# Kernel tuning notes

Hardware: AMD Instinct MI355X
Metric: run time of the kernel (lower is better)

The kernel has to match this reference:

```python
import jax, jax.numpy as jnp
import numpy as np

B, L, D_ENC = 32, 512, 512
STEPS = 32
E_DIM = 128      # embedding_dim
A_DIM = 256      # attention_dim
H = 512          # hidden_size
VOCAB = 32000


def _linear(x, W, b):
    return x @ W.T + b


def setup_inputs() -> dict:
    key = jax.random.key(0)
    ks = jax.random.split(key, 12)
    s = lambda fan_in: 1.0 / np.sqrt(fan_in)
    return {
        "encoder_outputs": jax.random.normal(ks[0], (B, L, D_ENC), dtype=jnp.float32),
        "target_seq": jax.random.randint(ks[1], (B, STEPS), 0, VOCAB, dtype=jnp.int64),
        "pos_embedding": jax.random.normal(ks[2], (STEPS, E_DIM), dtype=jnp.float32),
        "dec_proj_W": jax.random.uniform(ks[3], (A_DIM, E_DIM), minval=-s(E_DIM), maxval=s(E_DIM)),
        "dec_proj_b": jnp.zeros((A_DIM,), jnp.float32),
        "enc_proj_W": jax.random.uniform(ks[4], (A_DIM, D_ENC), minval=-s(D_ENC), maxval=s(D_ENC)),
        "enc_proj_b": jnp.zeros((A_DIM,), jnp.float32),
        "attn_score_W": jax.random.uniform(ks[5], (1, A_DIM), minval=-s(A_DIM), maxval=s(A_DIM)),
        "attn_score_b": jnp.zeros((1,), jnp.float32),
        "hidden_proj_W": jax.random.uniform(ks[6], (H, E_DIM), minval=-s(E_DIM), maxval=s(E_DIM)),
        "hidden_proj_b": jnp.zeros((H,), jnp.float32),
        "fc_out_W": jax.random.uniform(ks[7], (VOCAB, H + D_ENC), minval=-s(H + D_ENC), maxval=s(H + D_ENC)),
        "fc_out_b": jnp.zeros((VOCAB,), jnp.float32),
    }


def reference(encoder_outputs, target_seq, pos_embedding,
              dec_proj_W, dec_proj_b, enc_proj_W, enc_proj_b,
              attn_score_W, attn_score_b, hidden_proj_W, hidden_proj_b,
              fc_out_W, fc_out_b):
    batch = encoder_outputs.shape[0]
    steps = target_seq.shape[1]
    # [B, L, A]
    enc_proj = _linear(encoder_outputs, enc_proj_W, enc_proj_b)
    # [B, S, E]  (dropout=0 in eval)
    pos_emb = jnp.broadcast_to(pos_embedding[:steps][None], (batch, steps, pos_embedding.shape[1]))
    # [B, S, A]
    dec_query = _linear(pos_emb, dec_proj_W, dec_proj_b)
    # additive attention: [B, S, L, A]
    combined = jnp.tanh(enc_proj[:, None, :, :] + dec_query[:, :, None, :])
    # score reduction to scalar: [B, S, L]
    attn_scores = jnp.einsum('bsla,a->bsl', combined, attn_score_W[0]) + attn_score_b[0]
    attn_weights = jax.nn.softmax(attn_scores, axis=2)
    # context: [B, S, D_enc]
    context = jnp.einsum('bsl,bld->bsd', attn_weights, encoder_outputs)
    hidden = _linear(pos_emb, hidden_proj_W, hidden_proj_b)  # [B, S, H]
    logits = _linear(jnp.concatenate([hidden, context], axis=-1), fc_out_W, fc_out_b)
    return logits
```

## Files before the change

### kernel.cpp

```cpp
#include <hip/hip_runtime.h>
#include <hip/hip_bf16.h>
#include <stdint.h>

typedef __attribute__((ext_vector_type(4))) float f32x4;
typedef __attribute__((ext_vector_type(8))) short short8;

#define B_   32
#define L_   512
#define DE_  512
#define S_   32
#define ED_  128
#define AD_  256
#define HD_  512
#define VOC_ 32000
#define M_   1024

__device__ __forceinline__ unsigned short f2bf(float f){
  union { float f; unsigned int u; } v; v.f = f;
  unsigned int u = v.u;
  unsigned int r = (u + 0x7FFFu + ((u >> 16) & 1u)) >> 16;
  return (unsigned short)r;
}

__device__ __forceinline__ float bf2f(unsigned short u){
  union { unsigned int u; float f; } v; v.u = ((unsigned int)u) << 16;
  return v.f;
}

__device__ __forceinline__ float tanh_fast(float x){
  float t = __expf(2.0f * x);
  return (t - 1.0f) * __builtin_amdgcn_rcpf(t + 1.0f);
}

__device__ __forceinline__ void gl_lds16(const void* g, void* l){
  __builtin_amdgcn_global_load_lds(
      (const __attribute__((address_space(1))) unsigned int*)g,
      (__attribute__((address_space(3))) unsigned int*)l, 16, 0, 0);
}

extern "C" __global__ void __launch_bounds__(256)
k_cvt(const float* __restrict__ src, unsigned short* __restrict__ dst, int n4){
  int stride = gridDim.x * 256;
  for (int i = blockIdx.x * 256 + threadIdx.x; i < n4; i += stride){
    f32x4 v = ((const f32x4*)src)[i];
    ushort4 o;
    o.x = f2bf(v[0]); o.y = f2bf(v[1]); o.z = f2bf(v[2]); o.w = f2bf(v[3]);
    ((ushort4*)dst)[i] = o;
  }
}

extern "C" __global__ void __launch_bounds__(256)
k_small(const float* __restrict__ pos, const float* __restrict__ dW, const float* __restrict__ db,
        const float* __restrict__ hW, const float* __restrict__ hb,
        float* __restrict__ dq, unsigned short* __restrict__ hbf){
  int t = blockIdx.x * 256 + threadIdx.x;
  if (t < S_ * AD_){
    int s = t >> 8, a = t & 255;
    const float* p = pos + s * ED_;
    const float* wrow = dW + a * ED_;
    float acc = db[a];
    #pragma unroll 4
    for (int e = 0; e < ED_; ++e) acc += p[e] * wrow[e];
    dq[t] = acc;
  } else if (t < S_ * AD_ + S_ * HD_){
    int u = t - S_ * AD_;
    int s = u >> 9, h = u & 511;
    const float* p = pos + s * ED_;
    const float* wrow = hW + h * ED_;
    float acc = hb[h];
    #pragma unroll 4
    for (int e = 0; e < ED_; ++e) acc += p[e] * wrow[e];
    hbf[u] = f2bf(acc);
  }
}

extern "C" __global__ void __launch_bounds__(256)
k_gemm_encp(const unsigned short* __restrict__ A, const unsigned short* __restrict__ Bt,
            const float* __restrict__ bias, unsigned short* __restrict__ C){
  __shared__ unsigned short As[128 * 32];
  __shared__ unsigned short Bs[128 * 32];
  int bm = blockIdx.x >> 1, bn = blockIdx.x & 1;
  int tid = threadIdx.x, wid = tid >> 6, lane = tid & 63;
  int fr = lane & 15, fq = lane >> 4;
  int wm = wid >> 1, wn = wid & 1;
  f32x4 acc[4][4];
  #pragma unroll
  for (int i = 0; i < 4; ++i)
    #pragma unroll
    for (int j = 0; j < 4; ++j) acc[i][j] = (f32x4)0.0f;

  for (int k0 = 0; k0 < 512; k0 += 32){
    __syncthreads();
    #pragma unroll
    for (int i = 0; i < 2; ++i){
      int seg = wid * 2 + i;
      int row = seg * 16 + (lane >> 2);
      int col = (lane & 3) * 8;
      gl_lds16(A  + (size_t)(bm * 128 + row) * 512 + k0 + col, &As[seg * 512]);
      gl_lds16(Bt + (size_t)(bn * 128 + row) * 512 + k0 + col, &Bs[seg * 512]);
    }
    __syncthreads();
    short8 a[4], b[4];
    #pragma unroll
    for (int mf = 0; mf < 4; ++mf) a[mf] = *(const short8*)&As[(wm * 64 + mf * 16 + fr) * 32 + fq * 8];
    #pragma unroll
    for (int nf = 0; nf < 4; ++nf) b[nf] = *(const short8*)&Bs[(wn * 64 + nf * 16 + fr) * 32 + fq * 8];
    #pragma unroll
    for (int mf = 0; mf < 4; ++mf)
      #pragma unroll
      for (int nf = 0; nf < 4; ++nf)
        acc[mf][nf] = __builtin_amdgcn_mfma_f32_16x16x32_bf16(a[mf], b[nf], acc[mf][nf], 0, 0, 0);
  }
  #pragma unroll
  for (int mf = 0; mf < 4; ++mf){
    int row = bm * 128 + wm * 64 + mf * 16 + fq * 4;
    #pragma unroll
    for (int nf = 0; nf < 4; ++nf){
      int col = bn * 128 + wn * 64 + nf * 16 + fr;
      float bv = bias[col];
      #pragma unroll
      for (int j = 0; j < 4; ++j)
        C[(size_t)(row + j) * 256 + col] = f2bf(acc[mf][nf][j] + bv);
    }
  }
}

extern "C" __global__ void __launch_bounds__(256)
k_attn(const unsigned short* __restrict__ encp, const float* __restrict__ dq,
       const float* __restrict__ vW, float* __restrict__ wgt){
  int idx = blockIdx.x;
  int wg = (idx & 7) * 128 + (idx >> 3);
  int b = wg >> 5, s = wg & 31;
  int tid = threadIdx.x, wid = tid >> 6, lane = tid & 63;
  int half = lane >> 5, a0 = (lane & 31) * 8;
  __shared__ float sc[512];
  __shared__ float redm[4], reds[4];
  f32x4 dqa = *(const f32x4*)&dq[s * AD_ + a0];
  f32x4 dqb = *(const f32x4*)&dq[s * AD_ + a0 + 4];
  f32x4 va  = *(const f32x4*)&vW[a0];
  f32x4 vb  = *(const f32x4*)&vW[a0 + 4];
  for (int it = 0; it < 64; ++it){
    int l = wid * 128 + it * 2 + half;
    short8 e8 = *(const short8*)&encp[((size_t)(b * 512 + l)) * 256 + a0];
    float p = 0.0f;
    #pragma unroll
    for (int j = 0; j < 4; ++j) p += tanh_fast(bf2f((unsigned short)e8[j]) + dqa[j]) * va[j];
    #pragma unroll
    for (int j = 0; j < 4; ++j) p += tanh_fast(bf2f((unsigned short)e8[4 + j]) + dqb[j]) * vb[j];
    #pragma unroll
    for (int off = 16; off >= 1; off >>= 1) p += __shfl_xor(p, off);
    if ((lane & 31) == 0) sc[l] = p;
  }
  __syncthreads();
  float s0 = sc[tid], s1 = sc[tid + 256];
  float m = fmaxf(s0, s1);
  #pragma unroll
  for (int off = 32; off >= 1; off >>= 1) m = fmaxf(m, __shfl_xor(m, off));
  if (lane == 0) redm[wid] = m;
  __syncthreads();
  m = fmaxf(fmaxf(redm[0], redm[1]), fmaxf(redm[2], redm[3]));
  float e0 = __expf(s0 - m), e1 = __expf(s1 - m);
  float sum = e0 + e1;
  #pragma unroll
  for (int off = 32; off >= 1; off >>= 1) sum += __shfl_xor(sum, off);
  if (lane == 0) reds[wid] = sum;
  __syncthreads();
  float tot = reds[0] + reds[1] + reds[2] + reds[3];
  float inv = __builtin_amdgcn_rcpf(tot);
  size_t base = (size_t)(b * 32 + s) * 512;
  wgt[base + tid] = e0 * inv;
  wgt[base + tid + 256] = e1 * inv;
}

extern "C" __global__ void __launch_bounds__(256)
k_ctx(const unsigned short* __restrict__ encb, const float* __restrict__ wgt,
      unsigned short* __restrict__ ctx){
  int b = blockIdx.x >> 4, dt = blockIdx.x & 15;
  int tid = threadIdx.x;
  __shared__ float wl[32 * 512];
  #pragma unroll 8
  for (int i = 0; i < 64; ++i)
    wl[i * 256 + tid] = wgt[(size_t)b * 16384 + i * 256 + tid];
  __syncthreads();
  int d = dt * 32 + (tid & 31);
  int grp = tid >> 5;
  float acc0 = 0, acc1 = 0, acc2 = 0, acc3 = 0;
  const unsigned short* ebase = encb + (size_t)b * 262144 + d;
  const float* w0 = &wl[(grp * 4 + 0) * 512];
  const float* w1 = &wl[(grp * 4 + 1) * 512];
  const float* w2 = &wl[(grp * 4 + 2) * 512];
  const float* w3 = &wl[(grp * 4 + 3) * 512];
  #pragma unroll 8
  for (int l = 0; l < 512; ++l){
    float e = bf2f(ebase[(size_t)l * 512]);
    acc0 += w0[l] * e; acc1 += w1[l] * e; acc2 += w2[l] * e; acc3 += w3[l] * e;
  }
  size_t obase = (size_t)(b * 32 + grp * 4) * 512 + d;
  ctx[obase]        = f2bf(acc0);
  ctx[obase + 512]  = f2bf(acc1);
  ctx[obase + 1024] = f2bf(acc2);
  ctx[obase + 1536] = f2bf(acc3);
}

extern "C" __global__ void __launch_bounds__(256)
k_wprep(const float* __restrict__ fcW, const unsigned short* __restrict__ hbf,
        const float* __restrict__ fcb, unsigned short* __restrict__ Wc,
        float* __restrict__ logh){
  int bn = blockIdx.x;
  int tid = threadIdx.x, wid = tid >> 6, lane = tid & 63;
  int fr = lane & 15, fq = lane >> 4;
  #pragma unroll 8
  for (int i = 0; i < 32; ++i){
    int idx = i * 256 + tid;
    int row = idx >> 7, c4 = idx & 127;
    f32x4 v = *(const f32x4*)&fcW[(size_t)(bn * 64 + row) * 1024 + 512 + c4 * 4];
    ushort4 o;
    o.x = f2bf(v[0]); o.y = f2bf(v[1]); o.z = f2bf(v[2]); o.w = f2bf(v[3]);
    *(ushort4*)&Wc[(size_t)(bn * 64 + row) * 512 + c4 * 4] = o;
  }
  int col = bn * 64 + wid * 16 + fr;
  const float* brow = fcW + (size_t)col * 1024;
  f32x4 acc0 = (f32x4)0.0f, acc1 = (f32x4)0.0f;
  #pragma unroll 4
  for (int k0 = 0; k0 < 512; k0 += 32){
    int ko = k0 + fq * 8;
    f32x4 b0 = *(const f32x4*)(brow + ko);
    f32x4 b1 = *(const f32x4*)(brow + ko + 4);
    short8 bfr;
    bfr[0] = (short)f2bf(b0[0]); bfr[1] = (short)f2bf(b0[1]);
    bfr[2] = (short)f2bf(b0[2]); bfr[3] = (short)f2bf(b0[3]);
    bfr[4] = (short)f2bf(b1[0]); bfr[5] = (short)f2bf(b1[1]);
    bfr[6] = (short)f2bf(b1[2]); bfr[7] = (short)f2bf(b1[3]);
    short8 a0 = *(const short8*)&hbf[(size_t)fr * 512 + ko];
    short8 a1 = *(const short8*)&hbf[(size_t)(16 + fr) * 512 + ko];
    acc0 = __builtin_amdgcn_mfma_f32_16x16x32_bf16(a0, bfr, acc0, 0, 0, 0);
    acc1 = __builtin_amdgcn_mfma_f32_16x16x32_bf16(a1, bfr, acc1, 0, 0, 0);
  }
  float bv = fcb[col];
  #pragma unroll
  for (int j = 0; j < 4; ++j){
    logh[(size_t)(fq * 4 + j) * VOC_ + col]      = acc0[j] + bv;
    logh[(size_t)(16 + fq * 4 + j) * VOC_ + col] = acc1[j] + bv;
  }
}

extern "C" __global__ void __launch_bounds__(512, 2)
k_gemm_main(const unsigned short* __restrict__ Abf, const unsigned short* __restrict__ Wc,
            const float* __restrict__ logh, float* __restrict__ out){
  __shared__ unsigned short As[2][256 * 32];
  __shared__ unsigned short Bs[2][256 * 32];
  int orig = blockIdx.x;
  int xcd = orig & 7, j = orig >> 3;
  int wgid = (xcd < 4 ? xcd * 63 : 252 + (xcd - 4) * 62) + j;
  int bm = wgid & 3, bn = wgid >> 2;
  int tid = threadIdx.x, wid = tid >> 6, lane = tid & 63;
  int fr = lane & 15, fq = lane >> 4;
  int wm = wid >> 2, wn = wid & 3;
  int abase = bm * 256, bbase = bn * 256;
  int srow = lane >> 2;
  int scol = ((lane & 3) ^ ((lane >> 3) & 3)) * 8;
  int c0 = wid * 2;
  const unsigned short* aS0 = Abf + (size_t)(abase + c0 * 16 + srow) * 512 + scol;
  const unsigned short* aS1 = aS0 + (size_t)16 * 512;
  const unsigned short* bS0 = Wc  + (size_t)(bbase + c0 * 16 + srow) * 512 + scol;
  const unsigned short* bS1 = bS0 + (size_t)16 * 512;
  int swzfq = (fq ^ ((fr >> 1) & 3)) * 8;

  f32x4 acc[8][4];
  #pragma unroll
  for (int i = 0; i < 8; ++i)
    #pragma unroll
    for (int jj = 0; jj < 4; ++jj) acc[i][jj] = (f32x4)0.0f;

#define STAGE_MAIN(buf, kk) do { \
    gl_lds16(aS0 + (kk), &As[buf][c0 * 512]); \
    gl_lds16(aS1 + (kk), &As[buf][c0 * 512 + 512]); \
    gl_lds16(bS0 + (kk), &Bs[buf][c0 * 512]); \
    gl_lds16(bS1 + (kk), &Bs[buf][c0 * 512 + 512]); \
  } while (0)

  STAGE_MAIN(0, 0);
  __syncthreads();

  int cur = 0;
  for (int t = 0; t < 16; ++t){
    if (t < 15) STAGE_MAIN(cur ^ 1, (size_t)(t + 1) * 32);
    short8 a[8], b[4];
    #pragma unroll
    for (int mf = 0; mf < 8; ++mf)
      a[mf] = *(const short8*)&As[cur][(wm * 128 + mf * 16 + fr) * 32 + swzfq];
    #pragma unroll
    for (int nf = 0; nf < 4; ++nf)
      b[nf] = *(const short8*)&Bs[cur][(wn * 64 + nf * 16 + fr) * 32 + swzfq];
    #pragma unroll
    for (int mf = 0; mf < 8; ++mf)
      #pragma unroll
      for (int nf = 0; nf < 4; ++nf)
        acc[mf][nf] = __builtin_amdgcn_mfma_f32_16x16x32_bf16(a[mf], b[nf], acc[mf][nf], 0, 0, 0);
    __syncthreads();
    cur ^= 1;
  }
#undef STAGE_MAIN

  #pragma unroll
  for (int mf = 0; mf < 8; ++mf){
    int rowb = bm * 256 + wm * 128 + mf * 16 + fq * 4;
    #pragma unroll
    for (int nf = 0; nf < 4; ++nf){
      int col = bn * 256 + wn * 64 + nf * 16 + fr;
      #pragma unroll
      for (int jj = 0; jj < 4; ++jj){
        int r = rowb + jj;
        out[(size_t)r * VOC_ + col] = acc[mf][nf][jj] + logh[(size_t)(r & 31) * VOC_ + col];
      }
    }
  }
}

extern "C" void kernel_launch(void* const* d_in, const int* in_sizes, int n_in,
                              void* d_out, int out_size, void* d_ws, size_t ws_size,
                              hipStream_t stream){
  const float* enc = (const float*)d_in[0];
  const float* pos = (const float*)d_in[2];
  const float* dW  = (const float*)d_in[3];
  const float* db  = (const float*)d_in[4];
  const float* eW  = (const float*)d_in[5];
  const float* eb  = (const float*)d_in[6];
  const float* vW  = (const float*)d_in[7];
  const float* hW  = (const float*)d_in[9];
  const float* hb  = (const float*)d_in[10];
  const float* fcW = (const float*)d_in[11];
  const float* fcb = (const float*)d_in[12];
  float* out = (float*)d_out;

  char* w = (char*)d_ws;
  unsigned short* Wc_bf   = (unsigned short*)(w);
  unsigned short* enc_bf  = (unsigned short*)(w + 32768000);
  unsigned short* encp_bf = (unsigned short*)(w + 49545216);
  unsigned short* ctx     = (unsigned short*)(w + 57933824);
  float*          logh    = (float*)(w + 58982400);
  float*          dq      = (float*)(w + 63078400);
  unsigned short* hbf     = (unsigned short*)(w + 63111168);
  unsigned short* encW_bf = (unsigned short*)(w + 63143936);
  float*          wgt     = (float*)(w + 63406080);

  k_cvt<<<dim3(2048), dim3(256), 0, stream>>>(enc, enc_bf, 8388608 / 4);
  k_cvt<<<dim3(128), dim3(256), 0, stream>>>(eW, encW_bf, 131072 / 4);
  k_small<<<dim3(96), dim3(256), 0, stream>>>(pos, dW, db, hW, hb, dq, hbf);
  k_gemm_encp<<<dim3(256), dim3(256), 0, stream>>>(enc_bf, encW_bf, eb, encp_bf);
  k_attn<<<dim3(1024), dim3(256), 0, stream>>>(encp_bf, dq, vW, wgt);
  k_ctx<<<dim3(512), dim3(256), 0, stream>>>(enc_bf, wgt, ctx);
  k_wprep<<<dim3(500), dim3(256), 0, stream>>>(fcW, hbf, fcb, Wc_bf, logh);
  k_gemm_main<<<dim3(500), dim3(512), 0, stream>>>(ctx, Wc_bf, logh, out);
}
```

Before: 221.2 us.

## Triple-buffer B tiles and split MFMA loop with partial vmcnt waits

The main GEMM keeps double-buffered A in LDS but moves B to a three-deep buffer, so B is prefetched two K-steps ahead. Each K-step is split into two halves of MFMAs with the staging loads placed between them. Full __syncthreads is replaced by explicit s_waitcnt vmcnt and s_barrier, and s_setprio raises wave priority around the MFMA bursts. This aims to hide global-to-LDS latency and reduce barrier stalls, at the cost of extra LDS and hand-managed wait counts that must stay correct.

```diff
diff --git a/kernel.cpp b/kernel.cpp
--- a/kernel.cpp
+++ b/kernel.cpp
@@ -248,7 +248,7 @@
 k_gemm_main(const unsigned short* __restrict__ Abf, const unsigned short* __restrict__ Wc,
             const float* __restrict__ logh, float* __restrict__ out){
   __shared__ unsigned short As[2][256 * 32];
-  __shared__ unsigned short Bs[2][256 * 32];
+  __shared__ unsigned short Bs[3][256 * 32];
   int orig = blockIdx.x;
   int xcd = orig & 7, j = orig >> 3;
   int wgid = (xcd < 4 ? xcd * 63 : 252 + (xcd - 4) * 62) + j;
@@ -272,35 +272,60 @@
     #pragma unroll
     for (int jj = 0; jj < 4; ++jj) acc[i][jj] = (f32x4)0.0f;
 
-#define STAGE_MAIN(buf, kk) do { \
+#define STAGE_A(buf, kk) do { \
     gl_lds16(aS0 + (kk), &As[buf][c0 * 512]); \
     gl_lds16(aS1 + (kk), &As[buf][c0 * 512 + 512]); \
+  } while (0)
+#define STAGE_B(buf, kk) do { \
     gl_lds16(bS0 + (kk), &Bs[buf][c0 * 512]); \
     gl_lds16(bS1 + (kk), &Bs[buf][c0 * 512 + 512]); \
   } while (0)
 
-  STAGE_MAIN(0, 0);
-  __syncthreads();
-
-  int cur = 0;
+  STAGE_A(0, 0);
+  STAGE_B(0, 0);
+  STAGE_B(1, 32);
+  asm volatile("s_waitcnt vmcnt(2)" ::: "memory");
+  __builtin_amdgcn_s_barrier();
+  __builtin_amdgcn_sched_barrier(0);
+
+  #pragma unroll
   for (int t = 0; t < 16; ++t){
-    if (t < 15) STAGE_MAIN(cur ^ 1, (size_t)(t + 1) * 32);
+    const int ca = t & 1, cb = t % 3;
     short8 a[8], b[4];
-    #pragma unroll
-    for (int mf = 0; mf < 8; ++mf)
-      a[mf] = *(const short8*)&As[cur][(wm * 128 + mf * 16 + fr) * 32 + swzfq];
+    if (t < 15) STAGE_A(ca ^ 1, (size_t)(t + 1) * 32);
     #pragma unroll
     for (int nf = 0; nf < 4; ++nf)
-      b[nf] = *(const short8*)&Bs[cur][(wn * 64 + nf * 16 + fr) * 32 + swzfq];
-    #pragma unroll
-    for (int mf = 0; mf < 8; ++mf)
+      b[nf] = *(const short8*)&Bs[cb][(wn * 64 + nf * 16 + fr) * 32 + swzfq];
+    #pragma unroll
+    for (int mf = 0; mf < 4; ++mf)
+      a[mf] = *(const short8*)&As[ca][(wm * 128 + mf * 16 + fr) * 32 + swzfq];
+    __builtin_amdgcn_s_setprio(1);
+    #pragma unroll
+    for (int mf = 0; mf < 4; ++mf)
       #pragma unroll
       for (int nf = 0; nf < 4; ++nf)
         acc[mf][nf] = __builtin_amdgcn_mfma_f32_16x16x32_bf16(a[mf], b[nf], acc[mf][nf], 0, 0, 0);
-    __syncthreads();
-    cur ^= 1;
-  }
-#undef STAGE_MAIN
+    __builtin_amdgcn_s_setprio(0);
+    if (t < 14) STAGE_B((t + 2) % 3, (size_t)(t + 2) * 32);
+    #pragma unroll
+    for (int mf = 4; mf < 8; ++mf)
+      a[mf] = *(const short8*)&As[ca][(wm * 128 + mf * 16 + fr) * 32 + swzfq];
+    __builtin_amdgcn_s_setprio(1);
+    #pragma unroll
+    for (int mf = 4; mf < 8; ++mf)
+      #pragma unroll
+      for (int nf = 0; nf < 4; ++nf)
+        acc[mf][nf] = __builtin_amdgcn_mfma_f32_16x16x32_bf16(a[mf], b[nf], acc[mf][nf], 0, 0, 0);
+    __builtin_amdgcn_s_setprio(0);
+    if (t < 14)      asm volatile("s_waitcnt vmcnt(2)" ::: "memory");
+    else if (t == 14) asm volatile("s_waitcnt vmcnt(0)" ::: "memory");
+    if (t < 15){
+      __builtin_amdgcn_s_barrier();
+      __builtin_amdgcn_sched_barrier(0);
+    }
+  }
+#undef STAGE_A
+#undef STAGE_B
 
   #pragma unroll
   for (int mf = 0; mf < 8; ++mf){
```

Measured after the change: 210.6 us. -4.8%, faster.
